# Kernel optimization log

Hardware: AMD Instinct MI355X
Metric: run time of the kernel (lower is better)

## Reference

```python
import jax, jax.numpy as jnp
import numpy as np

NEG_SLOPE = 0.2
EPS_SOFTMAX = 1e-16
EPS_NORM = 1e-12
H = 4


def gat_conv(x, src, dst, edge_attr, W, att_src, att_dst, W_edge, att_edge, bias, concat):
    """PyG GATConv with edge_dim, add_self_loops=False.
    x: [N, F_in]; src,dst: [E]; edge_attr: [E, edge_dim]
    W: [F_in, H*C]; att_src/att_dst/att_edge: [H, C]; W_edge: [edge_dim, H*C]
    """
    N = x.shape[0]
    C = att_src.shape[1]
    xs = (x @ W).reshape(N, H, C)                      # [N,H,C]
    a_s = jnp.einsum('nhc,hc->nh', xs, att_src)        # [N,H]
    a_d = jnp.einsum('nhc,hc->nh', xs, att_dst)        # [N,H]
    e = (edge_attr @ W_edge).reshape(-1, H, C)         # [E,H,C]
    a_e = jnp.einsum('ehc,hc->eh', e, att_edge)        # [E,H]
    alpha = a_s[src] + a_d[dst] + a_e                  # [E,H]
    alpha = jax.nn.leaky_relu(alpha, NEG_SLOPE)
    # segment softmax over edges grouped by destination node
    m = jax.ops.segment_max(alpha, dst, num_segments=N)        # [N,H]
    ex = jnp.exp(alpha - m[dst])
    denom = jax.ops.segment_sum(ex, dst, num_segments=N)       # [N,H]
    alpha = ex / (denom[dst] + EPS_SOFTMAX)
    # message = attention-weighted source features, scatter-add to dst
    out = jax.ops.segment_sum(xs[src] * alpha[..., None], dst, num_segments=N)  # [N,H,C]
    out = out.reshape(N, H * C) if concat else out.mean(axis=1)
    return out + bias


def l2_normalize(x):
    n = jnp.linalg.norm(x, axis=-1, keepdims=True)
    return x / jnp.maximum(n, EPS_NORM)


def setup_inputs() -> dict:
    key = jax.random.key(0)
    ks = jax.random.split(key, 16)
    N, E, F_in, C1, C2 = 50000, 800000, 128, 64, 64
    glorot = lambda k, shape: jax.random.uniform(
        k, shape, jnp.float32, -1.0, 1.0) * np.sqrt(6.0 / (shape[0] + shape[-1]))
    return {
        'x': jax.random.normal(ks[0], (N, F_in), jnp.float32),
        'edge_index': jax.random.randint(ks[1], (2, E), 0, N, jnp.int32),
        'edge_weight': jax.random.uniform(ks[2], (E, 1), jnp.float32),
        # layer 1: in=128 -> H*C1=256, concat=True
        'W1': glorot(ks[3], (F_in, H * C1)),
        'att_src1': glorot(ks[4], (H, C1)),
        'att_dst1': glorot(ks[5], (H, C1)),
        'We1': glorot(ks[6], (1, H * C1)),
        'att_e1': glorot(ks[7], (H, C1)),
        'b1': jnp.zeros((H * C1,), jnp.float32),
        # layer 2: in=256 -> H*C2, concat=False (mean over heads)
        'W2': glorot(ks[8], (H * C1, H * C2)),
        'att_src2': glorot(ks[9], (H, C2)),
        'att_dst2': glorot(ks[10], (H, C2)),
        'We2': glorot(ks[11], (1, H * C2)),
        'att_e2': glorot(ks[12], (H, C2)),
        'b2': jnp.zeros((C2,), jnp.float32),
    }


def reference(x, edge_index, edge_weight, W1, att_src1, att_dst1, We1, att_e1, b1,
              W2, att_src2, att_dst2, We2, att_e2, b2):
    src, dst = edge_index[0], edge_index[1]
    h = gat_conv(x, src, dst, edge_weight, W1, att_src1, att_dst1, We1, att_e1, b1, concat=True)
    h = jax.nn.relu(l2_normalize(h))
    out = gat_conv(h, src, dst, edge_weight, W2, att_src2, att_dst2, We2, att_e2, b2, concat=False)
    return out
```

## Files before the change

kernel.cpp:

```cpp
#include <hip/hip_runtime.h>
#include <hip/hip_bf16.h>

typedef unsigned short u16;
typedef unsigned long long u64;
using bf16x8 = __attribute__((ext_vector_type(8))) short;
using f32x4v = __attribute__((ext_vector_type(4))) float;
typedef float v2f __attribute__((ext_vector_type(2)));

#define HC 256
#define CDIM 64

__device__ __forceinline__ float b2f(u16 u){
  union { unsigned int i; float f; } c; c.i = ((unsigned)u) << 16; return c.f;
}
__device__ __forceinline__ u16 f2b(float f){
  union { float f; unsigned int i; } c; c.f = f;
  unsigned int x = c.i;
  return (u16)((x + 0x7FFFu + ((x >> 16) & 1u)) >> 16);
}
__device__ __forceinline__ float ldf(const void* p, size_t i, int isbf){
  return isbf ? b2f(((const u16*)p)[i]) : ((const float*)p)[i];
}
__device__ __forceinline__ float sel4(float4 v, int h){ return h==0?v.x:(h==1?v.y:(h==2?v.z:v.w)); }
__device__ __forceinline__ float lrelu(float v){ return v>0.f ? v : 0.2f*v; }

__device__ __forceinline__ void glds16(const void* g, void* l){
  __builtin_amdgcn_global_load_lds(
      (const __attribute__((address_space(1))) unsigned int*)g,
      (__attribute__((address_space(3))) unsigned int*)l, 16, 0, 0);
}

__device__ __forceinline__ float4 wave_max4(float4 m){
  #pragma unroll
  for(int o=32;o>0;o>>=1){
    m.x=fmaxf(m.x,__shfl_xor(m.x,o));
    m.y=fmaxf(m.y,__shfl_xor(m.y,o));
    m.z=fmaxf(m.z,__shfl_xor(m.z,o));
    m.w=fmaxf(m.w,__shfl_xor(m.w,o));
  }
  return m;
}
__device__ __forceinline__ float4 wave_sum4(float4 m){
  #pragma unroll
  for(int o=32;o>0;o>>=1){
    m.x+=__shfl_xor(m.x,o);
    m.y+=__shfl_xor(m.y,o);
    m.z+=__shfl_xor(m.z,o);
    m.w+=__shfl_xor(m.w,o);
  }
  return m;
}

__global__ void k_hist(const int* __restrict__ dst, int E, int N, int* __restrict__ deg,
                       const u16* __restrict__ x, int nelem, int* __restrict__ flag){
  int e = blockIdx.x*256 + threadIdx.x;
  if (e < E){
    int d = dst[e];
    if ((unsigned)d < (unsigned)N) atomicAdd(&deg[d], 1);
  }
  if (blockIdx.x == 0){
    __shared__ int bad;
    if (threadIdx.x==0) bad = 0;
    __syncthreads();
    int n = nelem < 8192 ? nelem : 8192;
    int localbad = 0;
    for (int i=threadIdx.x; i<n; i+=256){
      int ex = (x[i] >> 7) & 0xFF;
      if (ex >= 140) localbad++;
    }
    if (localbad) atomicAdd(&bad, 1);
    __syncthreads();
    if (threadIdx.x==0) *flag = (bad==0) ? 1 : 0;
  }
}

__global__ void k_scan1(const int* __restrict__ in, int* __restrict__ out, int* __restrict__ bsums, int n){
  __shared__ int s[256];
  int t = threadIdx.x;
  int i = blockIdx.x*256 + t;
  int v = (i<n)? in[i] : 0;
  s[t]=v; __syncthreads();
  for(int off=1; off<256; off<<=1){
    int tv = (t>=off)? s[t-off] : 0;
    __syncthreads();
    s[t]+=tv; __syncthreads();
  }
  if (i<n) out[i] = s[t]-v;
  if (t==255) bsums[blockIdx.x] = s[255];
}

__global__ void k_scan2(int* __restrict__ bsums, int nb){
  __shared__ int s[256];
  int t=threadIdx.x;
  int v=(t<nb)? bsums[t]:0;
  s[t]=v; __syncthreads();
  for(int off=1; off<256; off<<=1){
    int tv=(t>=off)? s[t-off]:0;
    __syncthreads();
    s[t]+=tv; __syncthreads();
  }
  if (t<nb) bsums[t]=s[t]-v;
}

__global__ void k_scan3(int* __restrict__ out, const int* __restrict__ bsums, int n){
  int i = blockIdx.x*256+threadIdx.x;
  if (i<n) out[i]+=bsums[blockIdx.x];
}

__global__ void k_scatter(const int* __restrict__ src, const int* __restrict__ dst,
                          const void* __restrict__ ew, int E, int N,
                          const int* __restrict__ rowptr, int* __restrict__ cursor,
                          u64* __restrict__ epk,
                          const int* __restrict__ flagp){
  int e = blockIdx.x*256+threadIdx.x;
  if (e>=E) return;
  int bf = *flagp;
  int d = dst[e];
  if ((unsigned)d >= (unsigned)N) return;
  int p = rowptr[d] + atomicAdd(&cursor[d],1);
  int s = src[e];
  if ((unsigned)s >= (unsigned)N) s = 0;
  u64 v = ((u64)__float_as_uint(ldf(ew, e, bf)) << 32) | (unsigned)s;
  __builtin_nontemporal_store(v, &epk[p]);
}

__global__ void k_prep(const void* __restrict__ W1, const void* __restrict__ W2,
                       const void* __restrict__ We1, const void* __restrict__ ae1,
                       const void* __restrict__ We2, const void* __restrict__ ae2,
                       u16* __restrict__ Bt1, u16* __restrict__ Bt2, float* __restrict__ ce,
                       const int* __restrict__ flagp){
  int bf = *flagp;
  int b = blockIdx.x, t = threadIdx.x;
  if (b < 128){
    Bt1[(size_t)t*128 + b] = f2b(ldf(W1, (size_t)b*HC + t, bf));
  } else if (b < 384){
    int k = b - 128;
    Bt2[(size_t)t*256 + k] = f2b(ldf(W2, (size_t)k*HC + t, bf));
  } else {
    float p1 = ldf(We1, t, bf)*ldf(ae1, t, bf);
    float p2 = ldf(We2, t, bf)*ldf(ae2, t, bf);
    #pragma unroll
    for(int o=32;o>0;o>>=1){ p1+=__shfl_xor(p1,o); p2+=__shfl_xor(p2,o); }
    if((t&63)==0){ ce[t>>6]=p1; ce[4+(t>>6)]=p2; }
  }
}

__global__ __launch_bounds__(256) void k_gemm_mfma(
    const void* __restrict__ A, int a_ext, const u16* __restrict__ Bt,
    u16* __restrict__ C, const void* __restrict__ att_s, const void* __restrict__ att_d,
    float* __restrict__ a_s, float* __restrict__ a_d,
    int M, int K, const int* __restrict__ flagp)
{
  __shared__ u16 sh[64*264];
  __shared__ float att_sh[512];
  u16* As = sh;
  u16* Bs = sh + 2048;
  int bf = *flagp;
  int a_bf = a_ext ? bf : 1;
  int tid = threadIdx.x;
  int lane = tid & 63, w = tid >> 6;
  int quad = lane >> 4, ln = lane & 15;
  int m0 = blockIdx.x * 64;

  att_sh[tid]       = ldf(att_s, tid, bf);
  att_sh[256 + tid] = ldf(att_d, tid, bf);

  f32x4v acc[4][4] = {};
  for (int k0 = 0; k0 < K; k0 += 32){
    if (!a_ext){
      const u16* gA = (const u16*)A + (size_t)(m0 + (tid>>2))*K + k0 + (size_t)(tid&3)*8;
      glds16(gA, (char*)As + (size_t)w*1024);
    } else {
      int m = tid >> 2, g = tid & 3;
      int r = m0 + m;
      uint4 pack;
      if (r < M){
        size_t base = (size_t)r*K + k0 + g*8;
        if (a_bf){
          pack = *(const uint4*)((const u16*)A + base);
        } else {
          const float* Af = (const float*)A + base;
          float4 f0 = *(const float4*)Af;
          float4 f1 = *(const float4*)(Af+4);
          unsigned a0 = (unsigned)f2b(f0.x) | ((unsigned)f2b(f0.y)<<16);
          unsigned a1 = (unsigned)f2b(f0.z) | ((unsigned)f2b(f0.w)<<16);
          unsigned a2 = (unsigned)f2b(f1.x) | ((unsigned)f2b(f1.y)<<16);
          unsigned a3 = (unsigned)f2b(f1.z) | ((unsigned)f2b(f1.w)<<16);
          pack = make_uint4(a0,a1,a2,a3);
        }
      } else pack = make_uint4(0,0,0,0);
      ((uint4*)As)[tid] = pack;
    }
    #pragma unroll
    for (int i=0;i<4;i++){
      const u16* gB = Bt + (size_t)(i*64 + (tid>>2))*K + k0 + (size_t)(tid&3)*8;
      glds16(gB, (char*)Bs + (size_t)i*4096 + (size_t)w*1024);
    }
    __syncthreads();
    bf16x8 af[4], bfr[4];
    #pragma unroll
    for (int mi=0;mi<4;mi++) af[mi] = *(const bf16x8*)&As[(mi*16+ln)*32 + quad*8];
    #pragma unroll
    for (int nj=0;nj<4;nj++) bfr[nj] = *(const bf16x8*)&Bs[((size_t)w*64+nj*16+ln)*32 + quad*8];
    #pragma unroll
    for (int mi=0;mi<4;mi++)
      #pragma unroll
      for (int nj=0;nj<4;nj++)
        acc[mi][nj] = __builtin_amdgcn_mfma_f32_16x16x32_bf16(af[mi], bfr[nj], acc[mi][nj], 0,0,0);
    __syncthreads();
  }
  #pragma unroll
  for (int mi=0;mi<4;mi++)
    #pragma unroll
    for (int nj=0;nj<4;nj++){
      union { __hip_bfloat162 h2; u16 u[2]; } cv0, cv1;
      cv0.h2 = __float22bfloat162_rn(make_float2(acc[mi][nj][0], acc[mi][nj][1]));
      cv1.h2 = __float22bfloat162_rn(make_float2(acc[mi][nj][2], acc[mi][nj][3]));
      int col = w*64 + nj*16 + ln;
      int rbase = mi*16 + quad*4;
      sh[(rbase+0)*264 + col] = cv0.u[0];
      sh[(rbase+1)*264 + col] = cv0.u[1];
      sh[(rbase+2)*264 + col] = cv1.u[0];
      sh[(rbase+3)*264 + col] = cv1.u[1];
    }
  __syncthreads();
  #pragma unroll
  for (int j=0;j<8;j++){
    int idx = j*256 + tid;
    int r = idx >> 5, gq = idx & 31;
    if (m0 + r < M)
      *(uint4*)(C + (size_t)(m0+r)*HC + gq*8) = *(const uint4*)&sh[r*264 + gq*8];
  }
  {
    int r  = w*16 + ln;
    int hh = quad;
    const u16* crow = &sh[r*264 + hh*64];
    const float* asv = &att_sh[hh*64];
    const float* adv = &att_sh[256 + hh*64];
    float ps = 0.f, pd = 0.f;
    #pragma unroll
    for (int cb=0; cb<64; cb+=8){
      ushort4 ua = *(const ushort4*)&crow[cb];
      ushort4 ub = *(const ushort4*)&crow[cb+4];
      float4 sa = *(const float4*)&asv[cb];
      float4 sb = *(const float4*)&asv[cb+4];
      float4 da = *(const float4*)&adv[cb];
      float4 db = *(const float4*)&adv[cb+4];
      float c0=b2f(ua.x), c1=b2f(ua.y), c2=b2f(ua.z), c3=b2f(ua.w);
      float c4=b2f(ub.x), c5=b2f(ub.y), c6=b2f(ub.z), c7=b2f(ub.w);
      ps += c0*sa.x + c1*sa.y + c2*sa.z + c3*sa.w + c4*sb.x + c5*sb.y + c6*sb.z + c7*sb.w;
      pd += c0*da.x + c1*da.y + c2*da.z + c3*da.w + c4*db.x + c5*db.y + c6*db.z + c7*db.w;
    }
    if (m0 + r < M){
      a_s[(size_t)(m0+r)*4 + hh] = ps;
      a_d[(size_t)(m0+r)*4 + hh] = pd;
    }
  }
}

__global__ __launch_bounds__(256) void k_soft_agg(
    const u16* __restrict__ xs, const int* __restrict__ rowptr, const int* __restrict__ deg,
    const u64* __restrict__ epk,
    const float* __restrict__ a_s, const float* __restrict__ a_d, const float* __restrict__ ce4,
    const void* __restrict__ bias, void* __restrict__ outp, int N, int layer,
    const int* __restrict__ flagp){
  int bf = *flagp;
  int lane = threadIdx.x & 63;
  int w = threadIdx.x >> 6;
  int n = (blockIdx.x<<2) + w;
  if (n >= N) return;
  int row = rowptr[n];
  int dg = deg[n];
  float4 ad = *(const float4*)&a_d[(size_t)n*4];
  float4 ce = *(const float4*)ce4;
  int h = lane >> 4;
  float4 acc = make_float4(0.f,0.f,0.f,0.f);
  if (dg > 0){
    if (dg <= 64){
      int   s_reg = 0;
      float4 ar = make_float4(-1e30f,-1e30f,-1e30f,-1e30f);
      if (lane < dg){
        u64 pk = epk[row + lane];
        int s = (int)(unsigned)(pk & 0xFFFFFFFFull);
        if ((unsigned)s >= (unsigned)N) s = 0;
        s_reg = s;
        float wv = __uint_as_float((unsigned)(pk >> 32));
        float4 as = *(const float4*)&a_s[(size_t)s*4];
        ar.x = lrelu(as.x+ad.x+wv*ce.x);
        ar.y = lrelu(as.y+ad.y+wv*ce.y);
        ar.z = lrelu(as.z+ad.z+wv*ce.z);
        ar.w = lrelu(as.w+ad.w+wv*ce.w);
      }
      float4 m = wave_max4(ar);
      float4 ex = make_float4(0.f,0.f,0.f,0.f);
      if (lane < dg){
        ex.x=__expf(ar.x-m.x); ex.y=__expf(ar.y-m.y);
        ex.z=__expf(ar.z-m.z); ex.w=__expf(ar.w-m.w);
      }
      float4 ss = wave_sum4(ex);
      float4 wgt;
      wgt.x = ex.x/(ss.x+1e-16f); wgt.y = ex.y/(ss.y+1e-16f);
      wgt.z = ex.z/(ss.z+1e-16f); wgt.w = ex.w/(ss.w+1e-16f);
      float tw[4];
      #pragma unroll
      for (int j=0;j<4;j++){
        if (j*16 < dg){
          int srcl = j*16 + (lane & 15);
          float c0=__shfl(wgt.x,srcl), c1=__shfl(wgt.y,srcl);
          float c2=__shfl(wgt.z,srcl), c3=__shfl(wgt.w,srcl);
          tw[j] = (h==0)?c0:((h==1)?c1:((h==2)?c2:c3));
        } else tw[j] = 0.f;
      }
      int ibase = lane & 48;
      v2f a01 = {0.f,0.f}, a23 = {0.f,0.f};
      #pragma unroll
      for (int j=0;j<4;j++){
        int j0 = j*16;
        if (j0 >= dg) break;
        float twj = tw[j];
        int cnt = dg - j0; if (cnt > 16) cnt = 16;
        int t = 0;
        for (; t+4<=cnt; t+=4){
          int e = j0 + t;
          int s0=__builtin_amdgcn_readlane(s_reg,e+0);
          int s1=__builtin_amdgcn_readlane(s_reg,e+1);
          int s2=__builtin_amdgcn_readlane(s_reg,e+2);
          int s3=__builtin_amdgcn_readlane(s_reg,e+3);
          float w0=__shfl(twj, ibase+t+0);
          float w1=__shfl(twj, ibase+t+1);
          float w2=__shfl(twj, ibase+t+2);
          float w3=__shfl(twj, ibase+t+3);
          uint2 x0 = *(const uint2*)&xs[(size_t)s0*HC + lane*4];
          uint2 x1 = *(const uint2*)&xs[(size_t)s1*HC + lane*4];
          uint2 x2 = *(const uint2*)&xs[(size_t)s2*HC + lane*4];
          uint2 x3 = *(const uint2*)&xs[(size_t)s3*HC + lane*4];
          v2f f;
          f = (v2f){__uint_as_float(x0.x<<16), __uint_as_float(x0.x&0xFFFF0000u)}; a01 += f*w0;
          f = (v2f){__uint_as_float(x0.y<<16), __uint_as_float(x0.y&0xFFFF0000u)}; a23 += f*w0;
          f = (v2f){__uint_as_float(x1.x<<16), __uint_as_float(x1.x&0xFFFF0000u)}; a01 += f*w1;
          f = (v2f){__uint_as_float(x1.y<<16), __uint_as_float(x1.y&0xFFFF0000u)}; a23 += f*w1;
          f = (v2f){__uint_as_float(x2.x<<16), __uint_as_float(x2.x&0xFFFF0000u)}; a01 += f*w2;
          f = (v2f){__uint_as_float(x2.y<<16), __uint_as_float(x2.y&0xFFFF0000u)}; a23 += f*w2;
          f = (v2f){__uint_as_float(x3.x<<16), __uint_as_float(x3.x&0xFFFF0000u)}; a01 += f*w3;
          f = (v2f){__uint_as_float(x3.y<<16), __uint_as_float(x3.y&0xFFFF0000u)}; a23 += f*w3;
        }
        for (; t<cnt; t++){
          int s0=__builtin_amdgcn_readlane(s_reg,j0+t);
          float w0=__shfl(twj, ibase+t);
          uint2 x0 = *(const uint2*)&xs[(size_t)s0*HC + lane*4];
          v2f f;
          f = (v2f){__uint_as_float(x0.x<<16), __uint_as_float(x0.x&0xFFFF0000u)}; a01 += f*w0;
          f = (v2f){__uint_as_float(x0.y<<16), __uint_as_float(x0.y&0xFFFF0000u)}; a23 += f*w0;
        }
      }
      acc.x = a01.x; acc.y = a01.y; acc.z = a23.x; acc.w = a23.y;
    } else {
      float4 m = make_float4(-1e30f,-1e30f,-1e30f,-1e30f);
      for (int p=lane;p<dg;p+=64){
        u64 pk = epk[row+p];
        int s = (int)(unsigned)(pk & 0xFFFFFFFFull);
        if ((unsigned)s >= (unsigned)N) s = 0;
        float wv = __uint_as_float((unsigned)(pk >> 32));
        float4 as = *(const float4*)&a_s[(size_t)s*4];
        m.x=fmaxf(m.x, lrelu(as.x+ad.x+wv*ce.x));
        m.y=fmaxf(m.y, lrelu(as.y+ad.y+wv*ce.y));
        m.z=fmaxf(m.z, lrelu(as.z+ad.z+wv*ce.z));
        m.w=fmaxf(m.w, lrelu(as.w+ad.w+wv*ce.w));
      }
      m = wave_max4(m);
      float4 ss = make_float4(0.f,0.f,0.f,0.f);
      for (int p=lane;p<dg;p+=64){
        u64 pk = epk[row+p];
        int s = (int)(unsigned)(pk & 0xFFFFFFFFull);
        if ((unsigned)s >= (unsigned)N) s = 0;
        float wv = __uint_as_float((unsigned)(pk >> 32));
        float4 as = *(const float4*)&a_s[(size_t)s*4];
        ss.x+=__expf(lrelu(as.x+ad.x+wv*ce.x)-m.x);
        ss.y+=__expf(lrelu(as.y+ad.y+wv*ce.y)-m.y);
        ss.z+=__expf(lrelu(as.z+ad.z+wv*ce.z)-m.z);
        ss.w+=__expf(lrelu(as.w+ad.w+wv*ce.w)-m.w);
      }
      ss = wave_sum4(ss);
      float rsel=1.f/(sel4(ss,h)+1e-16f), mh=sel4(m,h), adh=sel4(ad,h), ceh=sel4(ce,h);
      for (int e=0;e<dg;e++){
        u64 pk = epk[row+e];
        int s = (int)(unsigned)(pk & 0xFFFFFFFFull);
        if ((unsigned)s >= (unsigned)N) s = 0;
        float wv = __uint_as_float((unsigned)(pk >> 32));
        float arv = lrelu(a_s[(size_t)s*4+h]+adh+wv*ceh);
        float wgt = __expf(arv-mh)*rsel;
        ushort4 xv4 = *(const ushort4*)&xs[(size_t)s*HC + lane*4];
        acc.x+=wgt*b2f(xv4.x); acc.y+=wgt*b2f(xv4.y);
        acc.z+=wgt*b2f(xv4.z); acc.w+=wgt*b2f(xv4.w);
      }
    }
  }
  if (layer==1){
    float4 v;
    v.x = acc.x + ldf(bias, lane*4+0, bf);
    v.y = acc.y + ldf(bias, lane*4+1, bf);
    v.z = acc.z + ldf(bias, lane*4+2, bf);
    v.w = acc.w + ldf(bias, lane*4+3, bf);
    float ss = v.x*v.x+v.y*v.y+v.z*v.z+v.w*v.w;
    #pragma unroll
    for(int o=32;o>0;o>>=1) ss += __shfl_xor(ss,o);
    float inv = 1.f/fmaxf(sqrtf(ss), 1e-12f);
    ushort4 o4;
    o4.x = f2b(fmaxf(v.x*inv,0.f)); o4.y = f2b(fmaxf(v.y*inv,0.f));
    o4.z = f2b(fmaxf(v.z*inv,0.f)); o4.w = f2b(fmaxf(v.w*inv,0.f));
    *(ushort4*)((u16*)outp + (size_t)n*HC + lane*4) = o4;
  } else {
    float4 s = acc;
    #pragma unroll
    for (int o=16;o<=32;o<<=1){
      s.x+=__shfl_xor(s.x,o); s.y+=__shfl_xor(s.y,o);
      s.z+=__shfl_xor(s.z,o); s.w+=__shfl_xor(s.w,o);
    }
    if (lane < 16){
      float4 v;
      v.x = 0.25f*s.x + ldf(bias, lane*4+0, bf);
      v.y = 0.25f*s.y + ldf(bias, lane*4+1, bf);
      v.z = 0.25f*s.z + ldf(bias, lane*4+2, bf);
      v.w = 0.25f*s.w + ldf(bias, lane*4+3, bf);
      if (bf){
        ushort4 o4; o4.x=f2b(v.x); o4.y=f2b(v.y); o4.z=f2b(v.z); o4.w=f2b(v.w);
        *(ushort4*)((u16*)outp + (size_t)n*CDIM + lane*4) = o4;
      } else {
        *(float4*)((float*)outp + (size_t)n*CDIM + lane*4) = v;
      }
    }
  }
}

extern "C" void kernel_launch(void* const* d_in, const int* in_sizes, int n_in,
                              void* d_out, int out_size, void* d_ws, size_t ws_size,
                              hipStream_t stream){
  const void* x_in = d_in[0];
  const int* eidx  = (const int*)d_in[1];
  const void* ew   = d_in[2];
  const void* W1   = d_in[3];
  const void* as1  = d_in[4];
  const void* ad1  = d_in[5];
  const void* We1  = d_in[6];
  const void* ae1  = d_in[7];
  const void* b1   = d_in[8];
  const void* W2   = d_in[9];
  const void* as2  = d_in[10];
  const void* ad2  = d_in[11];
  const void* We2  = d_in[12];
  const void* ae2  = d_in[13];
  const void* b2   = d_in[14];

  int N = in_sizes[0]/128;
  int E = in_sizes[2];
  const int* src = eidx;
  const int* dst = eidx + E;

  char* w = (char*)d_ws;
  auto alloc = [&](size_t bytes)->char*{ char* p=w; w += (bytes+255)/256*256; return p; };
  int*   flag  = (int*)alloc(256);
  u16*   xs    = (u16*)alloc((size_t)N*HC*2);
  u16*   agg   = (u16*)alloc((size_t)N*HC*2);
  float* a_s   = (float*)alloc((size_t)N*4*4);
  float* a_d   = (float*)alloc((size_t)N*4*4);
  int*   deg   = (int*)alloc((size_t)N*4);
  int*   cursor= (int*)alloc((size_t)N*4);
  int*   rowptr= (int*)alloc((size_t)N*4);
  int*   bsums = (int*)alloc(256*4);
  u64*   epk   = (u64*)alloc((size_t)E*8);
  float* ce    = (float*)alloc(256);
  u16*   Bt1   = (u16*)alloc((size_t)HC*128*2);
  u16*   Bt2   = (u16*)alloc((size_t)HC*HC*2);

  (void)hipMemsetAsync(deg, 0, (size_t)((char*)cursor - (char*)deg) + (size_t)N*4, stream);

  int eb = (E+255)/256;
  int nb = (N+255)/256;
  k_hist<<<eb,256,0,stream>>>(dst, E, N, deg, (const u16*)x_in, in_sizes[0], flag);
  k_scan1<<<nb,256,0,stream>>>(deg, rowptr, bsums, N);
  k_scan2<<<1,256,0,stream>>>(bsums, nb);
  k_scan3<<<nb,256,0,stream>>>(rowptr, bsums, N);
  k_scatter<<<eb,256,0,stream>>>(src, dst, ew, E, N, rowptr, cursor, epk, flag);
  k_prep<<<385,256,0,stream>>>(W1, W2, We1, ae1, We2, ae2, Bt1, Bt2, ce, flag);

  int gemmBlocks = (N+63)/64;
  int nwb = (N+3)/4;

  k_gemm_mfma<<<gemmBlocks,256,0,stream>>>(x_in, 1, Bt1, xs, as1, ad1, a_s, a_d, N, 128, flag);
  k_soft_agg<<<nwb,256,0,stream>>>(xs, rowptr, deg, epk, a_s, a_d, ce, b1, agg, N, 1, flag);

  k_gemm_mfma<<<gemmBlocks,256,0,stream>>>(agg, 0, Bt2, xs, as2, ad2, a_s, a_d, N, 256, flag);
  k_soft_agg<<<nwb,256,0,stream>>>(xs, rowptr, deg, epk, a_s, a_d, ce+4, b2, d_out, N, 2, flag);
}
```

Baseline: 369.5 us.

## Drop scan3 kernel by folding block offsets into consumers; widen GEMM K-tile to 64

Removes the third scan kernel, so scatter and the softmax-aggregation kernel add the per-block prefix offset (bsums[n>>8]) when they read rowptr. This saves one launch and one pass over rowptr at the cost of an extra small load in each consumer. The MFMA GEMM now stages 64-wide K tiles instead of 32, halving the number of sync-separated loop iterations and doing two MFMA halves per tile. This raises shared memory use per block.

```diff
diff --git a/kernel.cpp b/kernel.cpp
--- a/kernel.cpp
+++ b/kernel.cpp
@@ -102,22 +102,17 @@
   if (t<nb) bsums[t]=s[t]-v;
 }
 
-__global__ void k_scan3(int* __restrict__ out, const int* __restrict__ bsums, int n){
-  int i = blockIdx.x*256+threadIdx.x;
-  if (i<n) out[i]+=bsums[blockIdx.x];
-}
-
 __global__ void k_scatter(const int* __restrict__ src, const int* __restrict__ dst,
                           const void* __restrict__ ew, int E, int N,
-                          const int* __restrict__ rowptr, int* __restrict__ cursor,
-                          u64* __restrict__ epk,
+                          const int* __restrict__ rowptr, const int* __restrict__ bsums,
+                          int* __restrict__ cursor, u64* __restrict__ epk,
                           const int* __restrict__ flagp){
   int e = blockIdx.x*256+threadIdx.x;
   if (e>=E) return;
   int bf = *flagp;
   int d = dst[e];
   if ((unsigned)d >= (unsigned)N) return;
-  int p = rowptr[d] + atomicAdd(&cursor[d],1);
+  int p = rowptr[d] + bsums[d>>8] + atomicAdd(&cursor[d],1);
   int s = src[e];
   if ((unsigned)s >= (unsigned)N) s = 0;
   u64 v = ((u64)__float_as_uint(ldf(ew, e, bf)) << 32) | (unsigned)s;
@@ -151,10 +146,10 @@
     float* __restrict__ a_s, float* __restrict__ a_d,
     int M, int K, const int* __restrict__ flagp)
 {
-  __shared__ u16 sh[64*264];
+  __shared__ u16 sh[4096 + 16384];
   __shared__ float att_sh[512];
   u16* As = sh;
-  u16* Bs = sh + 2048;
+  u16* Bs = sh + 4096;
   int bf = *flagp;
   int a_bf = a_ext ? bf : 1;
   int tid = threadIdx.x;
@@ -166,47 +161,63 @@
   att_sh[256 + tid] = ldf(att_d, tid, bf);
 
   f32x4v acc[4][4] = {};
-  for (int k0 = 0; k0 < K; k0 += 32){
+  for (int k0 = 0; k0 < K; k0 += 64){
     if (!a_ext){
-      const u16* gA = (const u16*)A + (size_t)(m0 + (tid>>2))*K + k0 + (size_t)(tid&3)*8;
-      glds16(gA, (char*)As + (size_t)w*1024);
+      #pragma unroll
+      for (int j=0;j<2;j++){
+        int chunk = w*2 + j;
+        int r = m0 + chunk*8 + (lane>>3);
+        const u16* gA = (const u16*)A + (size_t)r*K + k0 + (lane&7)*8;
+        glds16(gA, (char*)As + chunk*1024);
+      }
     } else {
-      int m = tid >> 2, g = tid & 3;
-      int r = m0 + m;
-      uint4 pack;
+      int r = m0 + (tid>>2);
+      int kk = (tid&3)*16;
+      uint4 p0, p1;
       if (r < M){
-        size_t base = (size_t)r*K + k0 + g*8;
+        size_t base = (size_t)r*K + k0 + kk;
         if (a_bf){
-          pack = *(const uint4*)((const u16*)A + base);
+          p0 = *(const uint4*)((const u16*)A + base);
+          p1 = *(const uint4*)((const u16*)A + base + 8);
         } else {
           const float* Af = (const float*)A + base;
-          float4 f0 = *(const float4*)Af;
-          float4 f1 = *(const float4*)(Af+4);
-          unsigned a0 = (unsigned)f2b(f0.x) | ((unsigned)f2b(f0.y)<<16);
-          unsigned a1 = (unsigned)f2b(f0.z) | ((unsigned)f2b(f0.w)<<16);
-          unsigned a2 = (unsigned)f2b(f1.x) | ((unsigned)f2b(f1.y)<<16);
-          unsigned a3 = (unsigned)f2b(f1.z) | ((unsigned)f2b(f1.w)<<16);
-          pack = make_uint4(a0,a1,a2,a3);
+          float4 f0=*(const float4*)Af, f1=*(const float4*)(Af+4);
+          float4 f2=*(const float4*)(Af+8), f3=*(const float4*)(Af+12);
+          p0 = make_uint4((unsigned)f2b(f0.x)|((unsigned)f2b(f0.y)<<16),
+                          (unsigned)f2b(f0.z)|((unsigned)f2b(f0.w)<<16),
+                          (unsigned)f2b(f1.x)|((unsigned)f2b(f1.y)<<16),
+                          (unsigned)f2b(f1.z)|((unsigned)f2b(f1.w)<<16));
+          p1 = make_uint4((unsigned)f2b(f2.x)|((unsigned)f2b(f2.y)<<16),
+                          (unsigned)f2b(f2.z)|((unsigned)f2b(f2.w)<<16),
+                          (unsigned)f2b(f3.x)|((unsigned)f2b(f3.y)<<16),
+                          (unsigned)f2b(f3.z)|((unsigned)f2b(f3.w)<<16));
         }
-      } else pack = make_uint4(0,0,0,0);
-      ((uint4*)As)[tid] = pack;
-    }
-    #pragma unroll
-    for (int i=0;i<4;i++){
-      const u16* gB = Bt + (size_t)(i*64 + (tid>>2))*K + k0 + (size_t)(tid&3)*8;
-      glds16(gB, (char*)Bs + (size_t)i*4096 + (size_t)w*1024);
+      } else { p0 = make_uint4(0,0,0,0); p1 = p0; }
+      *(uint4*)&As[(size_t)tid*16]     = p0;
+      *(uint4*)&As[(size_t)tid*16 + 8] = p1;
+    }
+    #pragma unroll
+    for (int i=0;i<8;i++){
+      int chunk = w*8 + i;
+      int n = chunk*8 + (lane>>3);
+      const u16* gB = Bt + (size_t)n*K + k0 + (lane&7)*8;
+      glds16(gB, (char*)Bs + chunk*1024);
     }
     __syncthreads();
-    bf16x8 af[4], bfr[4];
-    #pragma unroll
-    for (int mi=0;mi<4;mi++) af[mi] = *(const bf16x8*)&As[(mi*16+ln)*32 + quad*8];
-    #pragma unroll
-    for (int nj=0;nj<4;nj++) bfr[nj] = *(const bf16x8*)&Bs[((size_t)w*64+nj*16+ln)*32 + quad*8];
-    #pragma unroll
-    for (int mi=0;mi<4;mi++)
+    #pragma unroll
+    for (int half=0; half<2; half++){
+      int ko = half*32 + quad*8;
+      bf16x8 af[4], bfr[4];
       #pragma unroll
-      for (int nj=0;nj<4;nj++)
-        acc[mi][nj] = __builtin_amdgcn_mfma_f32_16x16x32_bf16(af[mi], bfr[nj], acc[mi][nj], 0,0,0);
+      for (int mi=0;mi<4;mi++) af[mi] = *(const bf16x8*)&As[(mi*16+ln)*64 + ko];
+      #pragma unroll
+      for (int nj=0;nj<4;nj++) bfr[nj] = *(const bf16x8*)&Bs[(w*64+nj*16+ln)*64 + ko];
+      #pragma unroll
+      for (int mi=0;mi<4;mi++)
+        #pragma unroll
+        for (int nj=0;nj<4;nj++)
+          acc[mi][nj] = __builtin_amdgcn_mfma_f32_16x16x32_bf16(af[mi], bfr[nj], acc[mi][nj], 0,0,0);
+    }
     __syncthreads();
   }
   #pragma unroll
@@ -259,8 +270,8 @@
 }
 
 __global__ __launch_bounds__(256) void k_soft_agg(
-    const u16* __restrict__ xs, const int* __restrict__ rowptr, const int* __restrict__ deg,
-    const u64* __restrict__ epk,
+    const u16* __restrict__ xs, const int* __restrict__ rowptr, const int* __restrict__ bsums,
+    const int* __restrict__ deg, const u64* __restrict__ epk,
     const float* __restrict__ a_s, const float* __restrict__ a_d, const float* __restrict__ ce4,
     const void* __restrict__ bias, void* __restrict__ outp, int N, int layer,
     const int* __restrict__ flagp){
@@ -269,7 +280,7 @@
   int w = threadIdx.x >> 6;
   int n = (blockIdx.x<<2) + w;
   if (n >= N) return;
-  int row = rowptr[n];
+  int row = rowptr[n] + bsums[n>>8];
   int dg = deg[n];
   float4 ad = *(const float4*)&a_d[(size_t)n*4];
   float4 ce = *(const float4*)ce4;
@@ -479,16 +490,15 @@
   k_hist<<<eb,256,0,stream>>>(dst, E, N, deg, (const u16*)x_in, in_sizes[0], flag);
   k_scan1<<<nb,256,0,stream>>>(deg, rowptr, bsums, N);
   k_scan2<<<1,256,0,stream>>>(bsums, nb);
-  k_scan3<<<nb,256,0,stream>>>(rowptr, bsums, N);
-  k_scatter<<<eb,256,0,stream>>>(src, dst, ew, E, N, rowptr, cursor, epk, flag);
+  k_scatter<<<eb,256,0,stream>>>(src, dst, ew, E, N, rowptr, bsums, cursor, epk, flag);
   k_prep<<<385,256,0,stream>>>(W1, W2, We1, ae1, We2, ae2, Bt1, Bt2, ce, flag);
 
   int gemmBlocks = (N+63)/64;
   int nwb = (N+3)/4;
 
   k_gemm_mfma<<<gemmBlocks,256,0,stream>>>(x_in, 1, Bt1, xs, as1, ad1, a_s, a_d, N, 128, flag);
-  k_soft_agg<<<nwb,256,0,stream>>>(xs, rowptr, deg, epk, a_s, a_d, ce, b1, agg, N, 1, flag);
+  k_soft_agg<<<nwb,256,0,stream>>>(xs, rowptr, bsums, deg, epk, a_s, a_d, ce, b1, agg, N, 1, flag);
 
   k_gemm_mfma<<<gemmBlocks,256,0,stream>>>(agg, 0, Bt2, xs, as2, ad2, a_s, a_d, N, 256, flag);
-  k_soft_agg<<<nwb,256,0,stream>>>(xs, rowptr, deg, epk, a_s, a_d, ce+4, b2, d_out, N, 2, flag);
-}
+  k_soft_agg<<<nwb,256,0,stream>>>(xs, rowptr, bsums, deg, epk, a_s, a_d, ce+4, b2, d_out, N, 2, flag);
+}
```

Result: no change. 370.2 us (+0.2%).
